# Performance work log

Measured on AMD Instinct MI355X. Metric: run time of the kernel, lower is better.

The kernel has to match this reference:

```python
import jax, jax.numpy as jnp
import numpy as np

N = 8192
G = 12972
EPS = 1e-5


def setup_inputs() -> dict:
    key = jax.random.key(0)
    ks = jax.random.split(key, 8)
    # solutions: one-hot letters per position -> (N, 26, 5)
    sol_letters = jax.random.randint(ks[0], (N, 5), 0, 26)
    sols = jax.nn.one_hot(sol_letters, 26, dtype=jnp.float32).transpose(0, 2, 1)
    # guess vocabulary: one-hot words -> (G, 130) with (26,5) layout flattened
    g_letters = jax.random.randint(ks[1], (G, 5), 0, 26)
    guesses_mat = jax.nn.one_hot(g_letters, 26, dtype=jnp.float32).transpose(0, 2, 1).reshape(G, 130)
    s0 = 1.0 / np.sqrt(292.0)
    sh = 1.0 / np.sqrt(1000.0)
    W0 = jax.random.normal(ks[2], (292, 1000), jnp.float32) * s0
    b0 = jnp.zeros((1000,), jnp.float32)
    gammas = jnp.ones((4, 1000), jnp.float32)
    betas = jnp.zeros((4, 1000), jnp.float32)
    Wh = jax.random.normal(ks[3], (3, 1000, 1000), jnp.float32) * sh
    bh = jnp.zeros((3, 1000), jnp.float32)
    Wout = jax.random.normal(ks[4], (1000, 130), jnp.float32) * sh
    bout = jnp.zeros((130,), jnp.float32)
    return {"sols": sols, "guesses_mat": guesses_mat, "W0": W0, "b0": b0,
            "gammas": gammas, "betas": betas, "Wh": Wh, "bh": bh,
            "Wout": Wout, "bout": bout}


def _mlp(X, W0, b0, gammas, betas, Wh, bh, Wout, bout):
    h = X @ W0 + b0
    for i in range(4):
        mu = h.mean(axis=0)
        var = ((h - mu) ** 2).mean(axis=0)  # biased variance, as torch BN training
        h = gammas[i] * (h - mu) * jax.lax.rsqrt(var + EPS) + betas[i]
        h = jnp.where(h >= 0, h, 0.2 * h)
        if i < 3:
            h = h @ Wh[i] + bh[i]
        else:
            h = h @ Wout + bout
    return h


def reference(sols, guesses_mat, W0, b0, gammas, betas, Wh, bh, Wout, bout):
    n = sols.shape[0]
    hints = jnp.zeros((n, 286), jnp.float32)
    scores = 7.0 * jnp.ones((n,), jnp.float32)
    total_loss = jnp.float32(0.0)
    first_guess = None
    solved = jnp.zeros((n,), bool)
    sols_letters = jnp.clip(sols.sum(axis=2), 0.0, 1.0)[:, :, None]  # (n,26,1)
    for turn in range(6):
        turn_vec = jnp.zeros((n, 6), jnp.float32).at[:, turn].set(1.0)
        X = jnp.concatenate((hints, turn_vec), axis=1)  # (n, 292)
        y = _mlp(X, W0, b0, gammas, betas, Wh, bh, Wout, bout).reshape(n, 26, 5)
        logp = jax.nn.log_softmax(y, axis=1)
        loss = -(sols * logp).sum(axis=1).mean()
        if turn >= 1:
            total_loss = total_loss + loss
        y_soft = jax.nn.softmax(y, axis=1).reshape(n, 130)
        # nearest-guess retrieval: argmax over vocab of dot products, then gather
        sim = y_soft @ guesses_mat.T  # (n, G)
        idx = jnp.argmax(sim, axis=1)
        nudges = jax.lax.stop_gradient(guesses_mat[idx] - y_soft)
        guesses = (y_soft + nudges).reshape(n, 26, 5)
        if turn == 0:
            first_guess = guesses[0]
        greens = guesses * sols
        yellows = (1.0 - greens) * (guesses * sols_letters)
        blacks = (guesses * (1.0 - greens) * (1.0 - yellows)).sum(axis=2)  # (n,26)
        solved = greens.reshape(n, -1).sum(axis=1) == 5.0
        new_hints = jnp.concatenate((greens.reshape(n, 130), yellows.reshape(n, 130), blacks), axis=1)
        hints = hints + new_hints
        scores = jnp.where((scores > turn + 1) & solved, jnp.float32(turn + 1), scores)
    return total_loss, scores.sum(), solved.sum(), first_guess
```

## Files before the change

kernel.cpp:

```cpp
#include <hip/hip_runtime.h>

#define NROWS 8192
#define NG    12972
#define H     1000
#define NP    1024
#define KX    288
#define OCP   256
#define OC    130
#define EPSBN 1e-5f
#define MBLK  (NROWS / 128)

typedef __attribute__((ext_vector_type(8))) _Float16 f16x8;
typedef __attribute__((ext_vector_type(8))) unsigned short u16x8;
typedef __attribute__((ext_vector_type(4))) float f32x4;

__device__ __forceinline__ float lrelu(float x) { return x >= 0.f ? x : 0.2f * x; }

__global__ void transpose_f16(const float* __restrict__ src, int R, int C, int srcStride,
                              _Float16* __restrict__ dst, int Rp, int Cp) {
    __shared__ float tile[32][33];
    int k0 = blockIdx.x * 32;
    int n0 = blockIdx.y * 32;
    int tx = threadIdx.x, ty = threadIdx.y;
#pragma unroll
    for (int i = 0; i < 32; i += 8) {
        int k = k0 + ty + i, n = n0 + tx;
        tile[ty + i][tx] = (k < R && n < C) ? src[(size_t)k * srcStride + n] : 0.f;
    }
    __syncthreads();
#pragma unroll
    for (int i = 0; i < 32; i += 8) {
        int n = n0 + ty + i, k = k0 + tx;
        if (n < Cp && k < Rp) dst[(size_t)n * Rp + k] = (_Float16)tile[tx][ty + i];
    }
}

__global__ void prep_bias(const float* __restrict__ W0, const float* __restrict__ b0,
                          const float* __restrict__ bh, const float* __restrict__ bout,
                          float* __restrict__ b0p, float* __restrict__ w0t,
                          float* __restrict__ bhp, float* __restrict__ boutp) {
    int i = blockIdx.x * 256 + threadIdx.x;
    if (i < 1024) { b0p[i] = (i < H) ? b0[i] : 0.f; return; }
    i -= 1024;
    if (i < 6 * 1024) {
        int t = i >> 10, n = i & 1023;
        w0t[i] = (n < H) ? W0[(size_t)(286 + t) * H + n] : 0.f;
        return;
    }
    i -= 6 * 1024;
    if (i < 3 * 1024) {
        int l = i >> 10, n = i & 1023;
        bhp[i] = (n < H) ? bh[l * H + n] : 0.f;
        return;
    }
    i -= 3 * 1024;
    if (i < OCP) { boutp[i] = (i < OC) ? bout[i] : 0.f; }
}

__global__ void prep_guess_letters(const float* __restrict__ gm, unsigned char* __restrict__ gl,
                                   uint2* __restrict__ glp) {
    int g = blockIdx.x * blockDim.x + threadIdx.x;
    if (g >= NG) return;
    unsigned off[5];
    for (int p = 0; p < 5; ++p) {
        int letter = 0;
        for (int c = 0; c < 26; ++c)
            if (gm[(size_t)g * 130 + c * 5 + p] > 0.5f) { letter = c; break; }
        gl[g * 8 + p] = (unsigned char)letter;
        off[p] = (unsigned)(letter * 5 + p);
    }
    gl[g * 8 + 5] = gl[g * 8 + 6] = gl[g * 8 + 7] = 0;
    glp[g] = make_uint2(off[0] | (off[1] << 8) | (off[2] << 16) | (off[3] << 24), off[4]);
}

__global__ void prep_sol_letters(const float* __restrict__ sols, unsigned char* __restrict__ sl,
                                 unsigned int* __restrict__ msk) {
    int r = blockIdx.x * blockDim.x + threadIdx.x;
    if (r >= NROWS) return;
    unsigned int m = 0;
    for (int p = 0; p < 5; ++p) {
        int letter = 0;
        for (int c = 0; c < 26; ++c)
            if (sols[(size_t)r * 130 + c * 5 + p] > 0.5f) { letter = c; break; }
        sl[r * 8 + p] = (unsigned char)letter;
        m |= 1u << letter;
    }
    sl[r * 8 + 5] = sl[r * 8 + 6] = sl[r * 8 + 7] = 0;
    msk[r] = m;
}

__global__ void init_state(unsigned short* __restrict__ hX, float* __restrict__ scores,
                           int* __restrict__ solvedf, float* __restrict__ lossacc) {
    int i = blockIdx.x * blockDim.x + threadIdx.x;
    if (i < NROWS * KX) hX[i] = 0;
    if (i < NROWS) { scores[i] = 7.f; solvedf[i] = 0; }
    if (i == 0) lossacc[0] = 0.f;
}

template <int BK, bool HALF_C>
__global__ __launch_bounds__(256, 2) void gemm_f16(
    const _Float16* __restrict__ A, int lda,
    const _Float16* __restrict__ B, int ldb,
    void* __restrict__ Cv, int ldc,
    const float* __restrict__ bias1, const float* __restrict__ bias2, int kiter,
    float* __restrict__ pS, float* __restrict__ pS2) {
    constexpr int NCH = BK / 8;
    constexpr int ABYTES = 256 * BK;
    constexpr int KSUB = BK / 32;
    constexpr int AW = 16 * BK;
    __shared__ char smem[512 * BK];
    const int tid = threadIdx.x;
    const int lane = tid & 63;
    const int rowBase = blockIdx.x * 128;
    const int colBase = blockIdx.y * 128;
    const int wm = (tid >> 6) & 1;
    const int wn = tid >> 7;

    const _Float16* gsrc[NCH];
    int ldsuni[NCH];
#pragma unroll
    for (int i = 0; i < NCH; ++i) {
        int w = i * 256 + tid;
        const _Float16* plane;
        int off;
        if (w < AW) {
            int r = w & 127, kb = w >> 7;
            plane = A;
            off = (rowBase + r) * lda + kb * 8;
        } else {
            int v = w - AW;
            int col = v & 127, kb = v >> 7;
            plane = B;
            off = (colBase + col) * ldb + kb * 8;
        }
        gsrc[i] = plane + off;
        ldsuni[i] = (i * 256 + (tid & ~63)) * 16;
    }

    f32x4 acc[4][4];
    const f32x4 z = {0.f, 0.f, 0.f, 0.f};
#pragma unroll
    for (int m = 0; m < 4; ++m)
#pragma unroll
        for (int n = 0; n < 4; ++n) acc[m][n] = z;

    const int aro = (lane >> 4) * 2048 + (wm * 64 + (lane & 15)) * 16;
    const int bco = ABYTES + (lane >> 4) * 2048 + (wn * 64 + (lane & 15)) * 16;

    for (int t = 0; t < kiter; ++t) {
#pragma unroll
        for (int i = 0; i < NCH; ++i)
            __builtin_amdgcn_global_load_lds(
                (const __attribute__((address_space(1))) void*)(gsrc[i] + (size_t)t * BK),
                (__attribute__((address_space(3))) void*)(smem + ldsuni[i]), 16, 0, 0);
        __syncthreads();

        f16x8 a_f[KSUB][4], b_f[KSUB][4];
#pragma unroll
        for (int ks = 0; ks < KSUB; ++ks) {
#pragma unroll
            for (int m = 0; m < 4; ++m) a_f[ks][m] = *(const f16x8*)(smem + ks * 8192 + aro + m * 256);
#pragma unroll
            for (int n = 0; n < 4; ++n) b_f[ks][n] = *(const f16x8*)(smem + ks * 8192 + bco + n * 256);
        }
#pragma unroll
        for (int ks = 0; ks < KSUB; ++ks)
#pragma unroll
            for (int m = 0; m < 4; ++m)
#pragma unroll
                for (int n = 0; n < 4; ++n)
                    acc[m][n] = __builtin_amdgcn_mfma_f32_16x16x32_f16(a_f[ks][m], b_f[ks][n],
                                                                       acc[m][n], 0, 0, 0);
        __syncthreads();
    }

    float* sS  = (float*)smem;
    float* sS2 = (float*)smem + 256;
    const int lane16 = lane & 15, lanehi = lane >> 4;
#pragma unroll
    for (int n = 0; n < 4; ++n) {
        int col = colBase + wn * 64 + n * 16 + lane16;
        float bv = bias1[col] + (bias2 ? bias2[col] : 0.f);
        float s = 0.f, s2 = 0.f;
#pragma unroll
        for (int m = 0; m < 4; ++m) {
            int row0 = rowBase + wm * 64 + m * 16 + lanehi * 4;
#pragma unroll
            for (int r = 0; r < 4; ++r) {
                float cv = acc[m][n][r] + bv;
                if constexpr (HALF_C)
                    ((_Float16*)Cv)[(size_t)(row0 + r) * ldc + col] = (_Float16)cv;
                else
                    ((float*)Cv)[(size_t)(row0 + r) * ldc + col] = cv;
                s += cv; s2 += cv * cv;
            }
        }
        if (pS) {
            s += __shfl_xor(s, 16);  s += __shfl_xor(s, 32);
            s2 += __shfl_xor(s2, 16); s2 += __shfl_xor(s2, 32);
            if (lanehi == 0) {
                int lcol = wn * 64 + n * 16 + lane16;
                sS[wm * 128 + lcol] = s;
                sS2[wm * 128 + lcol] = s2;
            }
        }
    }
    if (pS) {
        __syncthreads();
        if (tid < 128) {
            int col = colBase + tid;
            pS[(size_t)blockIdx.x * NP + col] = sS[tid] + sS[128 + tid];
            pS2[(size_t)blockIdx.x * NP + col] = sS2[tid] + sS2[128 + tid];
        }
    }
}

__global__ __launch_bounds__(256, 2) void gemm_out64(
    const _Float16* __restrict__ A, int lda,
    const _Float16* __restrict__ B, int ldb,
    float* __restrict__ C, int ldc,
    const float* __restrict__ bias1, int kiter) {
    constexpr int BK = 64;
    __shared__ char smem[24576];
    const int tid = threadIdx.x;
    const int lane = tid & 63;
    const int rowBase = blockIdx.x * 64;
    const int colBase = blockIdx.y * 128;
    const int wn = tid >> 6;

    const _Float16* gsrc[6];
    int ldsuni[6];
#pragma unroll
    for (int i = 0; i < 6; ++i) {
        int w = i * 256 + tid;
        const _Float16* plane;
        int off;
        if (w < 512) {
            int r = w & 63, kb = w >> 6;
            plane = A;
            off = (rowBase + r) * lda + kb * 8;
        } else {
            int v = w - 512;
            int col = v & 127, kb = v >> 7;
            plane = B;
            off = (colBase + col) * ldb + kb * 8;
        }
        gsrc[i] = plane + off;
        ldsuni[i] = (i * 256 + (tid & ~63)) * 16;
    }

    f32x4 acc[4][2];
    const f32x4 z = {0.f, 0.f, 0.f, 0.f};
#pragma unroll
    for (int m = 0; m < 4; ++m)
#pragma unroll
        for (int n = 0; n < 2; ++n) acc[m][n] = z;

    const int aro = (lane >> 4) * 1024 + (lane & 15) * 16;
    const int bco = 8192 + (lane >> 4) * 2048 + (wn * 32 + (lane & 15)) * 16;

    for (int t = 0; t < kiter; ++t) {
#pragma unroll
        for (int i = 0; i < 6; ++i)
            __builtin_amdgcn_global_load_lds(
                (const __attribute__((address_space(1))) void*)(gsrc[i] + (size_t)t * BK),
                (__attribute__((address_space(3))) void*)(smem + ldsuni[i]), 16, 0, 0);
        __syncthreads();

        f16x8 a_f[2][4], b_f[2][2];
#pragma unroll
        for (int ks = 0; ks < 2; ++ks) {
#pragma unroll
            for (int m = 0; m < 4; ++m) a_f[ks][m] = *(const f16x8*)(smem + ks * 4096 + aro + m * 256);
#pragma unroll
            for (int n = 0; n < 2; ++n) b_f[ks][n] = *(const f16x8*)(smem + ks * 8192 + bco + n * 256);
        }
#pragma unroll
        for (int ks = 0; ks < 2; ++ks)
#pragma unroll
            for (int m = 0; m < 4; ++m)
#pragma unroll
                for (int n = 0; n < 2; ++n)
                    acc[m][n] = __builtin_amdgcn_mfma_f32_16x16x32_f16(a_f[ks][m], b_f[ks][n],
                                                                       acc[m][n], 0, 0, 0);
        __syncthreads();
    }

    const int lane16 = lane & 15, lanehi = lane >> 4;
#pragma unroll
    for (int n = 0; n < 2; ++n) {
        int col = colBase + wn * 32 + n * 16 + lane16;
        float bv = bias1[col];
#pragma unroll
        for (int m = 0; m < 4; ++m) {
            int row0 = rowBase + m * 16 + lanehi * 4;
#pragma unroll
            for (int r = 0; r < 4; ++r)
                C[(size_t)(row0 + r) * ldc + col] = acc[m][n][r] + bv;
        }
    }
}

__global__ __launch_bounds__(256) void bn_apply_f(
    const _Float16* __restrict__ hraw, const float* __restrict__ pS, const float* __restrict__ pS2,
    const float* __restrict__ gamma, const float* __restrict__ beta,
    _Float16* __restrict__ oh, int psjStride) {
    __shared__ float la[128], lb[128];
    const int tid = threadIdx.x;
    const int rowBase = blockIdx.x * 128;
    const int colBase = blockIdx.y * 128;
    if (tid < 128) {
        int col = colBase + tid;
        float s = 0.f;
        for (int j = 0; j < MBLK; ++j) s += pS[(size_t)j * psjStride + col];
        la[tid] = s;
    } else {
        int col = colBase + tid - 128;
        float s2 = 0.f;
        for (int j = 0; j < MBLK; ++j) s2 += pS2[(size_t)j * psjStride + col];
        lb[tid - 128] = s2;
    }
    __syncthreads();
    if (tid < 128) {
        int col = colBase + tid;
        float a = 0.f, b = 0.f;
        if (col < H) {
            float mean = la[tid] * (1.f / NROWS);
            float var = lb[tid] * (1.f / NROWS) - mean * mean;
            float inv = rsqrtf(var + EPSBN);
            a = gamma[col] * inv;
            b = beta[col] - mean * a;
        }
        la[tid] = a;
        lb[tid] = b;
    }
    __syncthreads();
    const int c8 = (tid & 15) * 8;
    float ar[8], br[8];
#pragma unroll
    for (int j = 0; j < 8; ++j) { ar[j] = la[c8 + j]; br[j] = lb[c8 + j]; }
#pragma unroll
    for (int i = 0; i < 8; ++i) {
        int row = i * 16 + (tid >> 4);
        const u16x8 v = *(const u16x8*)(hraw + (size_t)(rowBase + row) * NP + colBase + c8);
        u16x8 o;
#pragma unroll
        for (int j = 0; j < 8; ++j) {
            float x = (float)__builtin_bit_cast(_Float16, (unsigned short)v[j]);
            o[j] = __builtin_bit_cast(unsigned short, (_Float16)lrelu(ar[j] * x + br[j]));
        }
        *(u16x8*)((unsigned short*)oh + (size_t)(rowBase + row) * NP + colBase + c8) = o;
    }
}

__global__ __launch_bounds__(256) void post_turn(
    const float* __restrict__ ybuf, const uint2* __restrict__ glp,
    const unsigned char* __restrict__ gl, const unsigned char* __restrict__ sl,
    const unsigned int* __restrict__ msk, _Float16* __restrict__ hX,
    float* __restrict__ scores, int* __restrict__ solvedf, float* __restrict__ lossacc,
    const float* __restrict__ gm, float* __restrict__ dout, int turn) {
    const int r0 = blockIdx.x * 8;
    __shared__ float2 pk2[4][132];
    __shared__ float lcon[40];
    __shared__ float wb[4][8];
    __shared__ int wi[4][8];
    __shared__ int fidx[8];
    const int tid = threadIdx.x;

    if (tid < 40) {
        int row = tid / 5, p = tid - row * 5;
        const float* yr = ybuf + (size_t)(r0 + row) * OCP + p;
        float m = -1e30f;
#pragma unroll
        for (int c = 0; c < 26; ++c) m = fmaxf(m, yr[c * 5]);
        float e[26];
        float s = 0.f;
#pragma unroll
        for (int c = 0; c < 26; ++c) { e[c] = expf(yr[c * 5] - m); s += e[c]; }
        float inv = 1.f / s;
#pragma unroll
        for (int c = 0; c < 26; ++c)
            ((float*)&pk2[row >> 1][c * 5 + p])[row & 1] = e[c] * inv;
        lcon[tid] = logf(s) + m - yr[sl[(size_t)(r0 + row) * 8 + p] * 5];
    }
    __syncthreads();

    float bb[8];
    int ii[8];
#pragma unroll
    for (int r = 0; r < 8; ++r) { bb[r] = -1e30f; ii[r] = 1 << 30; }
    for (int g = tid; g < NG; g += 256) {
        uint2 w = glp[g];
        int o0 = w.x & 255, o1 = (w.x >> 8) & 255, o2 = (w.x >> 16) & 255,
            o3 = w.x >> 24, o4 = w.y & 255;
#pragma unroll
        for (int tp = 0; tp < 4; ++tp) {
            float2 s0 = pk2[tp][o0];
            float2 s1 = pk2[tp][o1];
            float2 s2 = pk2[tp][o2];
            float2 s3 = pk2[tp][o3];
            float2 s4 = pk2[tp][o4];
            float vx = s0.x + s1.x; vx += s2.x; vx += s3.x; vx += s4.x;
            float vy = s0.y + s1.y; vy += s2.y; vy += s3.y; vy += s4.y;
            if (vx > bb[2 * tp]) { bb[2 * tp] = vx; ii[2 * tp] = g; }
            if (vy > bb[2 * tp + 1]) { bb[2 * tp + 1] = vy; ii[2 * tp + 1] = g; }
        }
    }
#pragma unroll
    for (int off = 1; off < 64; off <<= 1) {
#pragma unroll
        for (int r = 0; r < 8; ++r) {
            float o = __shfl_xor(bb[r], off);
            int oi = __shfl_xor(ii[r], off);
            if (o > bb[r] || (o == bb[r] && oi < ii[r])) { bb[r] = o; ii[r] = oi; }
        }
    }
    const int wid = tid >> 6, lane = tid & 63;
    if (lane == 0) {
#pragma unroll
        for (int r = 0; r < 8; ++r) { wb[wid][r] = bb[r]; wi[wid][r] = ii[r]; }
    }
    __syncthreads();

    if (tid < 8) {
        float b = wb[0][tid]; int x = wi[0][tid];
#pragma unroll
        for (int wv = 1; wv < 4; ++wv)
            if (wb[wv][tid] > b || (wb[wv][tid] == b && wi[wv][tid] < x)) { b = wb[wv][tid]; x = wi[wv][tid]; }
        fidx[tid] = x;
        int r = r0 + tid;
        const unsigned char* q = gl + x * 8;
        const unsigned char* so = sl + (size_t)r * 8;
        unsigned int mk = msk[r];
        _Float16* hrow = hX + (size_t)r * KX;
        int allg = 1;
#pragma unroll
        for (int p = 0; p < 5; ++p) {
            int g = q[p];
            int off;
            if (g == so[p]) {
                off = g * 5 + p;
            } else {
                allg = 0;
                off = ((mk >> g) & 1u) ? (130 + g * 5 + p) : (260 + g);
            }
            hrow[off] = (_Float16)((float)hrow[off] + 1.f);
        }
        solvedf[r] = allg;
        if (allg && scores[r] > (float)(turn + 1)) scores[r] = (float)(turn + 1);
    }
    if (tid == 16 && turn >= 1) {
        float t = 0.f;
#pragma unroll
        for (int j = 0; j < 40; ++j) t += lcon[j];
        atomicAdd(lossacc, t * (1.f / (NROWS * 5)));
    }
    __syncthreads();
    if (turn == 0 && blockIdx.x == 0 && tid >= 64 && tid < 64 + OC) {
        dout[3 + tid - 64] = gm[(size_t)fidx[0] * OC + (tid - 64)];
    }
}

__global__ __launch_bounds__(256) void post_turn0(
    const float* __restrict__ ybuf, const uint2* __restrict__ glp,
    const float* __restrict__ gm, float* __restrict__ dout, int* __restrict__ idx0buf) {
    __shared__ float pk[132];
    __shared__ float wb[4];
    __shared__ int wi[4];
    __shared__ int fidx;
    const int tid = threadIdx.x;
    if (tid < 5) {
        int p = tid;
        const float* yr = ybuf + p;
        float m = -1e30f;
#pragma unroll
        for (int c = 0; c < 26; ++c) m = fmaxf(m, yr[c * 5]);
        float e[26];
        float s = 0.f;
#pragma unroll
        for (int c = 0; c < 26; ++c) { e[c] = expf(yr[c * 5] - m); s += e[c]; }
        float inv = 1.f / s;
#pragma unroll
        for (int c = 0; c < 26; ++c) pk[c * 5 + p] = e[c] * inv;
    }
    __syncthreads();
    float b = -1e30f;
    int bi = 1 << 30;
    for (int g = tid; g < NG; g += 256) {
        uint2 w = glp[g];
        int o0 = w.x & 255, o1 = (w.x >> 8) & 255, o2 = (w.x >> 16) & 255,
            o3 = w.x >> 24, o4 = w.y & 255;
        float v = pk[o0] + pk[o1]; v += pk[o2]; v += pk[o3]; v += pk[o4];
        if (v > b) { b = v; bi = g; }
    }
#pragma unroll
    for (int off = 1; off < 64; off <<= 1) {
        float o = __shfl_xor(b, off);
        int oi = __shfl_xor(bi, off);
        if (o > b || (o == b && oi < bi)) { b = o; bi = oi; }
    }
    const int wid = tid >> 6, lane = tid & 63;
    if (lane == 0) { wb[wid] = b; wi[wid] = bi; }
    __syncthreads();
    if (tid == 0) {
        float bx = wb[0]; int x = wi[0];
#pragma unroll
        for (int wv = 1; wv < 4; ++wv)
            if (wb[wv] > bx || (wb[wv] == bx && wi[wv] < x)) { bx = wb[wv]; x = wi[wv]; }
        fidx = x;
        idx0buf[0] = x;
    }
    __syncthreads();
    if (tid >= 64 && tid < 64 + OC) {
        dout[3 + tid - 64] = gm[(size_t)fidx * OC + (tid - 64)];
    }
}

__global__ void hints0(const int* __restrict__ idx0buf, const unsigned char* __restrict__ gl,
                       const unsigned char* __restrict__ sl, const unsigned int* __restrict__ msk,
                       _Float16* __restrict__ hX, float* __restrict__ scores,
                       int* __restrict__ solvedf) {
    int r = blockIdx.x * 256 + threadIdx.x;
    if (r >= NROWS) return;
    int x = idx0buf[0];
    const unsigned char* q = gl + x * 8;
    const unsigned char* so = sl + (size_t)r * 8;
    unsigned int mk = msk[r];
    _Float16* hrow = hX + (size_t)r * KX;
    int allg = 1;
#pragma unroll
    for (int p = 0; p < 5; ++p) {
        int g = q[p];
        int off;
        if (g == so[p]) {
            off = g * 5 + p;
        } else {
            allg = 0;
            off = ((mk >> g) & 1u) ? (130 + g * 5 + p) : (260 + g);
        }
        hrow[off] = (_Float16)((float)hrow[off] + 1.f);
    }
    solvedf[r] = allg;
    if (allg && scores[r] > 1.f) scores[r] = 1.f;
}

__global__ void final_reduce(const float* __restrict__ scores, const int* __restrict__ solvedf,
                             const float* __restrict__ lossacc, float* __restrict__ dout) {
    __shared__ float rs[256];
    __shared__ int ri[256];
    int tid = threadIdx.x;
    float s = 0.f;
    int c = 0;
    for (int r = tid; r < NROWS; r += 256) { s += scores[r]; c += solvedf[r]; }
    rs[tid] = s; ri[tid] = c;
    __syncthreads();
    for (int off = 128; off > 0; off >>= 1) {
        if (tid < off) { rs[tid] += rs[tid + off]; ri[tid] += ri[tid + off]; }
        __syncthreads();
    }
    if (tid == 0) {
        dout[0] = lossacc[0];
        dout[1] = rs[0];
        dout[2] = (float)ri[0];
    }
}

extern "C" void kernel_launch(void* const* d_in, const int* in_sizes, int n_in,
                              void* d_out, int out_size, void* d_ws, size_t ws_size,
                              hipStream_t stream) {
    const float* sols   = (const float*)d_in[0];
    const float* gm     = (const float*)d_in[1];
    const float* W0     = (const float*)d_in[2];
    const float* b0     = (const float*)d_in[3];
    const float* gammas = (const float*)d_in[4];
    const float* betas  = (const float*)d_in[5];
    const float* Wh     = (const float*)d_in[6];
    const float* bh     = (const float*)d_in[7];
    const float* Wout   = (const float*)d_in[8];
    const float* bout   = (const float*)d_in[9];
    float* dout = (float*)d_out;

    char* p = (char*)d_ws;
    auto alloc = [&](size_t bytes) { void* r = (void*)p; p += (bytes + 255) & ~(size_t)255; return r; };
    _Float16* hX   = (_Float16*)alloc((size_t)NROWS * KX * 2);
    _Float16* hA   = (_Float16*)alloc((size_t)NROWS * NP * 2);
    _Float16* hraw = (_Float16*)alloc((size_t)NROWS * NP * 2);
    float* ybuf    = (float*)alloc((size_t)NROWS * OCP * 4);
    _Float16* B0T = (_Float16*)alloc((size_t)NP * KX * 2);
    _Float16* WhT = (_Float16*)alloc((size_t)3 * NP * NP * 2);
    _Float16* BoT = (_Float16*)alloc((size_t)OCP * NP * 2);
    float* b0p   = (float*)alloc(NP * 4);
    float* w0t   = (float*)alloc(6 * NP * 4);
    float* bhp   = (float*)alloc(3 * NP * 4);
    float* boutp = (float*)alloc(OCP * 4);
    float* pS    = (float*)alloc((size_t)MBLK * NP * 4);
    float* pS2   = (float*)alloc((size_t)MBLK * NP * 4);
    float* scores  = (float*)alloc(NROWS * 4);
    float* lossacc = (float*)alloc(256);
    int* solvedf = (int*)alloc(NROWS * 4);
    int* idx0buf = (int*)alloc(256);
    unsigned char* gl = (unsigned char*)alloc(NG * 8);
    uint2* glp = (uint2*)alloc(NG * 8);
    unsigned char* sl = (unsigned char*)alloc(NROWS * 8);
    unsigned int* msk = (unsigned int*)alloc(NROWS * 4);

    transpose_f16<<<dim3(KX / 32, NP / 32), dim3(32, 8), 0, stream>>>(W0, 286, H, H, B0T, KX, NP);
    for (int l = 0; l < 3; ++l)
        transpose_f16<<<dim3(NP / 32, NP / 32), dim3(32, 8), 0, stream>>>(
            Wh + (size_t)l * H * H, H, H, H, WhT + (size_t)l * NP * NP, NP, NP);
    transpose_f16<<<dim3(NP / 32, OCP / 32), dim3(32, 8), 0, stream>>>(Wout, H, OC, OC, BoT, NP, OCP);
    prep_bias<<<41, 256, 0, stream>>>(W0, b0, bh, bout, b0p, w0t, bhp, boutp);
    prep_guess_letters<<<(NG + 255) / 256, 256, 0, stream>>>(gm, gl, glp);
    prep_sol_letters<<<(NROWS + 255) / 256, 256, 0, stream>>>(sols, sl, msk);
    init_state<<<(NROWS * KX + 255) / 256, 256, 0, stream>>>((unsigned short*)hX, scores, solvedf, lossacc);

    for (int t = 0; t < 6; ++t) {
        const int mg = (t == 0) ? 1 : MBLK;
        const int psStride = (t == 0) ? 0 : NP;
        gemm_f16<32, true><<<dim3(mg, NP / 128), 256, 0, stream>>>(
            hX, KX, B0T, KX, hraw, NP, b0p, w0t + t * NP, KX / 32, pS, pS2);
        for (int l = 0; l < 4; ++l) {
            bn_apply_f<<<dim3(mg, NP / 128), 256, 0, stream>>>(
                hraw, pS, pS2, gammas + (size_t)l * H, betas + (size_t)l * H, hA, psStride);
            if (l < 3) {
                gemm_f16<64, true><<<dim3(mg, NP / 128), 256, 0, stream>>>(
                    hA, NP, WhT + (size_t)l * NP * NP, NP, hraw, NP, bhp + l * NP, nullptr,
                    NP / 64, pS, pS2);
            } else {
                gemm_out64<<<dim3((t == 0) ? 1 : MBLK * 2, OCP / 128), 256, 0, stream>>>(
                    hA, NP, BoT, NP, ybuf, OCP, boutp, NP / 64);
            }
        }
        if (t == 0) {
            post_turn0<<<1, 256, 0, stream>>>(ybuf, glp, gm, dout, idx0buf);
            hints0<<<NROWS / 256, 256, 0, stream>>>(idx0buf, gl, sl, msk, hX, scores, solvedf);
        } else {
            post_turn<<<NROWS / 8, 256, 0, stream>>>(ybuf, glp, gl, sl, msk, hX, scores, solvedf,
                                                     lossacc, gm, dout, t);
        }
    }
    final_reduce<<<1, 256, 0, stream>>>(scores, solvedf, lossacc, dout);
}
```

Baseline: 1.539 ms.

## Add XCD-aware block swizzle to GEMMs and unpack post_turn score table

Adds a block-index remap so that consecutive tiles land on the same XCD, which should improve L2 reuse of the shared A/B panels in both GEMM kernels. Separately, post_turn's paired float2 softmax table becomes a plain per-row float table, and the guess scan now does scalar LDS reads per row instead of 64-bit paired reads. The LDS change doubles the number of LDS load instructions in the hot guess loop, which may cost more than the simpler layout saves.

```diff
diff --git a/kernel.cpp b/kernel.cpp
--- a/kernel.cpp
+++ b/kernel.cpp
@@ -15,6 +15,18 @@
 typedef __attribute__((ext_vector_type(4))) float f32x4;
 
 __device__ __forceinline__ float lrelu(float x) { return x >= 0.f ? x : 0.2f * x; }
+
+__device__ __forceinline__ void xcd_swz(int& bx, int& by) {
+    int nx = gridDim.x;
+    int nwg = nx * gridDim.y;
+    if ((nwg & 7) == 0) {
+        int bid = by * nx + bx;
+        int cpx = nwg >> 3;
+        int s = (bid & 7) * cpx + (bid >> 3);
+        bx = s % nx;
+        by = s / nx;
+    }
+}
 
 __global__ void transpose_f16(const float* __restrict__ src, int R, int C, int srcStride,
                               _Float16* __restrict__ dst, int Rp, int Cp) {
@@ -111,8 +123,11 @@
     __shared__ char smem[512 * BK];
     const int tid = threadIdx.x;
     const int lane = tid & 63;
-    const int rowBase = blockIdx.x * 128;
-    const int colBase = blockIdx.y * 128;
+    int bx = blockIdx.x, by = blockIdx.y;
+    xcd_swz(bx, by);
+    const int rowBase = bx * 128;
+    const int colBase = by * 128;
+    const int bidx = bx;
     const int wm = (tid >> 6) & 1;
     const int wn = tid >> 7;
 
@@ -209,8 +224,8 @@
         __syncthreads();
         if (tid < 128) {
             int col = colBase + tid;
-            pS[(size_t)blockIdx.x * NP + col] = sS[tid] + sS[128 + tid];
-            pS2[(size_t)blockIdx.x * NP + col] = sS2[tid] + sS2[128 + tid];
+            pS[(size_t)bidx * NP + col] = sS[tid] + sS[128 + tid];
+            pS2[(size_t)bidx * NP + col] = sS2[tid] + sS2[128 + tid];
         }
     }
 }
@@ -224,8 +239,10 @@
     __shared__ char smem[24576];
     const int tid = threadIdx.x;
     const int lane = tid & 63;
-    const int rowBase = blockIdx.x * 64;
-    const int colBase = blockIdx.y * 128;
+    int bx = blockIdx.x, by = blockIdx.y;
+    xcd_swz(bx, by);
+    const int rowBase = bx * 64;
+    const int colBase = by * 128;
     const int wn = tid >> 6;
 
     const _Float16* gsrc[6];
@@ -360,7 +377,7 @@
     float* __restrict__ scores, int* __restrict__ solvedf, float* __restrict__ lossacc,
     const float* __restrict__ gm, float* __restrict__ dout, int turn) {
     const int r0 = blockIdx.x * 8;
-    __shared__ float2 pk2[4][132];
+    __shared__ float pk[8][132];
     __shared__ float lcon[40];
     __shared__ float wb[4][8];
     __shared__ int wi[4][8];
@@ -379,8 +396,7 @@
         for (int c = 0; c < 26; ++c) { e[c] = expf(yr[c * 5] - m); s += e[c]; }
         float inv = 1.f / s;
 #pragma unroll
-        for (int c = 0; c < 26; ++c)
-            ((float*)&pk2[row >> 1][c * 5 + p])[row & 1] = e[c] * inv;
+        for (int c = 0; c < 26; ++c) pk[row][c * 5 + p] = e[c] * inv;
         lcon[tid] = logf(s) + m - yr[sl[(size_t)(r0 + row) * 8 + p] * 5];
     }
     __syncthreads();
@@ -394,16 +410,9 @@
         int o0 = w.x & 255, o1 = (w.x >> 8) & 255, o2 = (w.x >> 16) & 255,
             o3 = w.x >> 24, o4 = w.y & 255;
 #pragma unroll
-        for (int tp = 0; tp < 4; ++tp) {
-            float2 s0 = pk2[tp][o0];
-            float2 s1 = pk2[tp][o1];
-            float2 s2 = pk2[tp][o2];
-            float2 s3 = pk2[tp][o3];
-            float2 s4 = pk2[tp][o4];
-            float vx = s0.x + s1.x; vx += s2.x; vx += s3.x; vx += s4.x;
-            float vy = s0.y + s1.y; vy += s2.y; vy += s3.y; vy += s4.y;
-            if (vx > bb[2 * tp]) { bb[2 * tp] = vx; ii[2 * tp] = g; }
-            if (vy > bb[2 * tp + 1]) { bb[2 * tp + 1] = vy; ii[2 * tp + 1] = g; }
+        for (int r = 0; r < 8; ++r) {
+            float v = pk[r][o0] + pk[r][o1]; v += pk[r][o2]; v += pk[r][o3]; v += pk[r][o4];
+            if (v > bb[r]) { bb[r] = v; ii[r] = g; }
         }
     }
 #pragma unroll
```

Result: no change. 1.510 ms (-1.9%).
